# Kernel optimization log

Hardware: AMD Instinct MI355X
Metric: run time of the kernel (lower is better)

## Reference

```python
import jax, jax.numpy as jnp
import numpy as np

B, D, P = 1024, 1024, 16  # batch, latent_dim(=out_dim), part_dim

def setup_inputs() -> dict:
    key = jax.random.key(0)
    k1, k2 = jax.random.split(key)
    x = jax.random.normal(k1, (B, D, P), dtype=jnp.float32)
    # per-part Linear weights, torch Linear weight shape [out, in] stacked over parts
    W = jax.random.normal(k2, (P, D, D), dtype=jnp.float32) * 0.02
    return {"x": x, "W": W}

def reference(x, W):
    # x: [B, D, P]; W: [P, O, D] (O == D here). stack_dim=-1: slice last dim,
    # apply part-specific Linear (no bias) + exact GELU, stack on last dim.
    y = jnp.einsum('bdp,pod->bop', x, W)  # grouped per-part GEMM -> [B, O, P]
    return jax.nn.gelu(y, approximate=False)
```

## Files before the change

### kernel.cpp

```cpp
#include <hip/hip_runtime.h>
#include <hip/hip_bf16.h>
#include <math.h>

typedef __hip_bfloat16 bf16;
typedef __attribute__((ext_vector_type(8))) short bf16x8;
typedef __attribute__((ext_vector_type(4))) float f32x4;

#define DI static __device__ __forceinline__

constexpr int NB = 1024;
constexpr int ND = 1024;
constexpr int NP = 16;
constexpr int BK = 32;

DI float gelu_exact(float x) {
    return 0.5f * x * (1.0f + erff(x * 0.70710678118654752f));
}

__global__ __launch_bounds__(256) void pack_x_kernel(const float* __restrict__ x,
                                                     bf16* __restrict__ xp) {
    const int b = blockIdx.x;
    const int t = threadIdx.x;
    const int p = t & 15;
    const int dg = t >> 4;
    const float* xb = x + (size_t)b * ND * NP;
    bf16* dst = xp + (size_t)p * NB * ND + (size_t)b * ND;
#pragma unroll
    for (int c = 0; c < 8; ++c) {
        const int d0 = dg * 64 + c * 8;
        alignas(16) bf16 tmp[8];
#pragma unroll
        for (int j = 0; j < 8; ++j)
            tmp[j] = __float2bfloat16(xb[(size_t)(d0 + j) * NP + p]);
        *reinterpret_cast<bf16x8*>(&dst[d0]) = *reinterpret_cast<const bf16x8*>(tmp);
    }
}

__global__ __launch_bounds__(256) void pack_w_kernel(const float* __restrict__ w,
                                                     bf16* __restrict__ wp) {
    const size_t i = ((size_t)blockIdx.x * 256 + threadIdx.x) * 8;
    const float4 f0 = *reinterpret_cast<const float4*>(&w[i]);
    const float4 f1 = *reinterpret_cast<const float4*>(&w[i + 4]);
    alignas(16) bf16 tmp[8] = { __float2bfloat16(f0.x), __float2bfloat16(f0.y),
                                __float2bfloat16(f0.z), __float2bfloat16(f0.w),
                                __float2bfloat16(f1.x), __float2bfloat16(f1.y),
                                __float2bfloat16(f1.z), __float2bfloat16(f1.w) };
    *reinterpret_cast<bf16x8*>(&wp[i]) = *reinterpret_cast<const bf16x8*>(tmp);
}

template<bool DIRECT>
__global__ __launch_bounds__(256, 2) void gemm_kernel(const bf16* __restrict__ xp,
                                                      const bf16* __restrict__ wp,
                                                      float* __restrict__ yout) {
    __shared__ bf16 As[2][128 * BK];
    __shared__ bf16 Bs[2][128 * BK];
    const int p  = blockIdx.z;
    const int bt = blockIdx.y * 128;
    const int ot = blockIdx.x * 128;
    const bf16* A  = xp + (size_t)p * NB * ND;
    const bf16* Bm = wp + (size_t)p * ND * ND;
    const int t = threadIdx.x;
    const int l = t & 63;
    const int w = t >> 6;
    const int wr = w >> 1, wc = w & 1;

    f32x4 acc[4][4] = {};

    auto stage = [&](int buf, int k0) {
#pragma unroll
        for (int r = 0; r < 2; ++r) {
            const int c   = r * 256 + t;
            const int row = c >> 2;
            const int cc  = c & 3;
            const bf16* ga = A  + (size_t)(bt + row) * ND + (k0 + cc * 8);
            const bf16* gb = Bm + (size_t)(ot + row) * ND + (k0 + cc * 8);
            bf16* la = &As[buf][(r * 256 + w * 64) * 8];
            bf16* lb = &Bs[buf][(r * 256 + w * 64) * 8];
            __builtin_amdgcn_global_load_lds((const __attribute__((address_space(1))) void*)ga,
                                             (__attribute__((address_space(3))) void*)la, 16, 0, 0);
            __builtin_amdgcn_global_load_lds((const __attribute__((address_space(1))) void*)gb,
                                             (__attribute__((address_space(3))) void*)lb, 16, 0, 0);
        }
    };

    int buf = 0;
    stage(0, 0);
    const int NK = ND / BK;
    for (int kt = 0; kt < NK; ++kt) {
        __syncthreads();
        if (kt + 1 < NK) stage(buf ^ 1, (kt + 1) * BK);
        const int lr = l & 15;
        const int lk = (l >> 4) * 8;
        bf16x8 af[4], bf_[4];
#pragma unroll
        for (int m = 0; m < 4; ++m)
            af[m] = *reinterpret_cast<const bf16x8*>(&As[buf][(wr * 64 + m * 16 + lr) * BK + lk]);
#pragma unroll
        for (int n = 0; n < 4; ++n)
            bf_[n] = *reinterpret_cast<const bf16x8*>(&Bs[buf][(wc * 64 + n * 16 + lr) * BK + lk]);
#pragma unroll
        for (int m = 0; m < 4; ++m)
#pragma unroll
            for (int n = 0; n < 4; ++n)
                acc[m][n] = __builtin_amdgcn_mfma_f32_16x16x32_bf16(af[m], bf_[n], acc[m][n], 0, 0, 0);
        buf ^= 1;
    }

    const int lr4 = (l >> 4) * 4;
    const int lc  = l & 15;
    const int row0 = bt + wr * 64, col0 = ot + wc * 64;
#pragma unroll
    for (int m = 0; m < 4; ++m) {
#pragma unroll
        for (int j = 0; j < 4; ++j) {
            const int r = row0 + m * 16 + lr4 + j;
#pragma unroll
            for (int n = 0; n < 4; ++n) {
                const int c = col0 + n * 16 + lc;
                const float v = acc[m][n][j];
                if (DIRECT) {
                    yout[((size_t)r * ND + c) * NP + p] = gelu_exact(v);
                } else {
                    yout[(size_t)p * NB * ND + (size_t)r * ND + c] = v;
                }
            }
        }
    }
}

__global__ __launch_bounds__(256) void unpack_gelu_kernel(const float* __restrict__ y,
                                                          float* __restrict__ out) {
    const size_t f = (size_t)blockIdx.x * 256 + threadIdx.x;
    const int    p0 = (int)(f & 3) * 4;
    const size_t o  = (f >> 2) & 1023;
    const size_t b  = f >> 12;
    const float* yb = y + b * (size_t)ND + o;
    float4 v;
    v.x = gelu_exact(yb[(size_t)(p0 + 0) * (NB * ND)]);
    v.y = gelu_exact(yb[(size_t)(p0 + 1) * (NB * ND)]);
    v.z = gelu_exact(yb[(size_t)(p0 + 2) * (NB * ND)]);
    v.w = gelu_exact(yb[(size_t)(p0 + 3) * (NB * ND)]);
    reinterpret_cast<float4*>(out)[f] = v;
}

__global__ __launch_bounds__(256) void fallback_kernel(const float* __restrict__ x,
                                                       const float* __restrict__ w,
                                                       float* __restrict__ out) {
    __shared__ float As[64][17];
    __shared__ float Bs[64][17];
    const int p = blockIdx.z, bt = blockIdx.y * 64, ot = blockIdx.x * 64;
    const int t = threadIdx.x;
    const int tx = t & 15, ty = t >> 4;
    float acc[4][4] = {};
    for (int k0 = 0; k0 < ND; k0 += 16) {
        __syncthreads();
#pragma unroll
        for (int i = 0; i < 4; ++i) {
            const int idx = i * 256 + t;
            const int r = idx >> 4, k = idx & 15;
            As[r][k] = x[((size_t)(bt + r) * ND + k0 + k) * NP + p];
            Bs[r][k] = w[(size_t)p * ND * ND + (size_t)(ot + r) * ND + k0 + k];
        }
        __syncthreads();
#pragma unroll
        for (int k = 0; k < 16; ++k) {
            float a[4], bb[4];
#pragma unroll
            for (int i = 0; i < 4; ++i) a[i] = As[ty * 4 + i][k];
#pragma unroll
            for (int j = 0; j < 4; ++j) bb[j] = Bs[tx * 4 + j][k];
#pragma unroll
            for (int i = 0; i < 4; ++i)
#pragma unroll
                for (int j = 0; j < 4; ++j) acc[i][j] += a[i] * bb[j];
        }
    }
#pragma unroll
    for (int i = 0; i < 4; ++i)
#pragma unroll
        for (int j = 0; j < 4; ++j)
            out[((size_t)(bt + ty * 4 + i) * ND + (ot + tx * 4 + j)) * NP + p] =
                gelu_exact(acc[i][j]);
}

extern "C" void kernel_launch(void* const* d_in, const int* in_sizes, int n_in,
                              void* d_out, int out_size, void* d_ws, size_t ws_size,
                              hipStream_t stream) {
    const float* x = (const float*)d_in[0];
    const float* w = (const float*)d_in[1];
    float* out = (float*)d_out;

    const size_t nElem     = (size_t)NP * NB * ND;
    const size_t packBytes = nElem * sizeof(bf16) * 2;
    const size_t yBytes    = nElem * sizeof(float);

    if (ws_size >= packBytes) {
        bf16* xp = (bf16*)d_ws;
        bf16* wp = xp + nElem;
        pack_x_kernel<<<NB, 256, 0, stream>>>(x, xp);
        pack_w_kernel<<<(int)(nElem / (256 * 8)), 256, 0, stream>>>(w, wp);
        if (ws_size >= packBytes + yBytes) {
            float* y = (float*)((char*)d_ws + packBytes);
            gemm_kernel<false><<<dim3(8, 8, 16), 256, 0, stream>>>(xp, wp, y);
            unpack_gelu_kernel<<<(int)(nElem / (256 * 4)), 256, 0, stream>>>(y, out);
        } else {
            gemm_kernel<true><<<dim3(8, 8, 16), 256, 0, stream>>>(xp, wp, out);
        }
    } else {
        fallback_kernel<<<dim3(16, 16, 16), 256, 0, stream>>>(x, w, out);
    }
}
```

Before: 134.8 us.

## Fuse GELU into GEMM, store bf16 intermediate, remap block order, raise occupancy

Moves the exact GELU into the GEMM epilogue and writes the intermediate as bf16 instead of fp32, halving the bytes the GEMM writes and the unpack kernel reads. The grid is flattened to 1D with a remap that interleaves parts across consecutive blocks, presumably to spread L2/channel traffic, and launch bounds are raised to 4 blocks per CU. The bf16 intermediate adds an extra rounding of the output, and the higher occupancy target may force register spills.

```diff
diff --git a/kernel.cpp b/kernel.cpp
--- a/kernel.cpp
+++ b/kernel.cpp
@@ -48,15 +48,17 @@
     *reinterpret_cast<bf16x8*>(&wp[i]) = *reinterpret_cast<const bf16x8*>(tmp);
 }
 
-template<bool DIRECT>
-__global__ __launch_bounds__(256, 2) void gemm_kernel(const bf16* __restrict__ xp,
+template<bool YBF>
+__global__ __launch_bounds__(256, 4) void gemm_kernel(const bf16* __restrict__ xp,
                                                       const bf16* __restrict__ wp,
-                                                      float* __restrict__ yout) {
+                                                      void* __restrict__ yout) {
     __shared__ bf16 As[2][128 * BK];
     __shared__ bf16 Bs[2][128 * BK];
-    const int p  = blockIdx.z;
-    const int bt = blockIdx.y * 128;
-    const int ot = blockIdx.x * 128;
+    const int i = blockIdx.x;
+    const int p    = ((i & 7) << 1) | ((i >> 9) & 1);
+    const int tile = (i >> 3) & 63;
+    const int ot = (tile & 7) * 128;
+    const int bt = (tile >> 3) * 128;
     const bf16* A  = xp + (size_t)p * NB * ND;
     const bf16* Bm = wp + (size_t)p * ND * ND;
     const int t = threadIdx.x;
@@ -117,29 +119,30 @@
 #pragma unroll
             for (int n = 0; n < 4; ++n) {
                 const int c = col0 + n * 16 + lc;
-                const float v = acc[m][n][j];
-                if (DIRECT) {
-                    yout[((size_t)r * ND + c) * NP + p] = gelu_exact(v);
+                const float v = gelu_exact(acc[m][n][j]);
+                if (YBF) {
+                    ((bf16*)yout)[(size_t)p * NB * ND + (size_t)r * ND + c] =
+                        __float2bfloat16(v);
                 } else {
-                    yout[(size_t)p * NB * ND + (size_t)r * ND + c] = v;
+                    ((float*)yout)[((size_t)r * ND + c) * NP + p] = v;
                 }
             }
         }
     }
 }
 
-__global__ __launch_bounds__(256) void unpack_gelu_kernel(const float* __restrict__ y,
-                                                          float* __restrict__ out) {
+__global__ __launch_bounds__(256) void unpack_kernel(const bf16* __restrict__ y,
+                                                     float* __restrict__ out) {
     const size_t f = (size_t)blockIdx.x * 256 + threadIdx.x;
     const int    p0 = (int)(f & 3) * 4;
     const size_t o  = (f >> 2) & 1023;
     const size_t b  = f >> 12;
-    const float* yb = y + b * (size_t)ND + o;
+    const bf16* yb = y + b * (size_t)ND + o;
     float4 v;
-    v.x = gelu_exact(yb[(size_t)(p0 + 0) * (NB * ND)]);
-    v.y = gelu_exact(yb[(size_t)(p0 + 1) * (NB * ND)]);
-    v.z = gelu_exact(yb[(size_t)(p0 + 2) * (NB * ND)]);
-    v.w = gelu_exact(yb[(size_t)(p0 + 3) * (NB * ND)]);
+    v.x = __bfloat162float(yb[(size_t)(p0 + 0) * (NB * ND)]);
+    v.y = __bfloat162float(yb[(size_t)(p0 + 1) * (NB * ND)]);
+    v.z = __bfloat162float(yb[(size_t)(p0 + 2) * (NB * ND)]);
+    v.w = __bfloat162float(yb[(size_t)(p0 + 3) * (NB * ND)]);
     reinterpret_cast<float4*>(out)[f] = v;
 }
 
@@ -192,7 +195,7 @@
 
     const size_t nElem     = (size_t)NP * NB * ND;
     const size_t packBytes = nElem * sizeof(bf16) * 2;
-    const size_t yBytes    = nElem * sizeof(float);
+    const size_t yBytes    = nElem * sizeof(bf16);
 
     if (ws_size >= packBytes) {
         bf16* xp = (bf16*)d_ws;
@@ -200,11 +203,11 @@
         pack_x_kernel<<<NB, 256, 0, stream>>>(x, xp);
         pack_w_kernel<<<(int)(nElem / (256 * 8)), 256, 0, stream>>>(w, wp);
         if (ws_size >= packBytes + yBytes) {
-            float* y = (float*)((char*)d_ws + packBytes);
-            gemm_kernel<false><<<dim3(8, 8, 16), 256, 0, stream>>>(xp, wp, y);
-            unpack_gelu_kernel<<<(int)(nElem / (256 * 4)), 256, 0, stream>>>(y, out);
+            bf16* y = (bf16*)((char*)d_ws + packBytes);
+            gemm_kernel<true><<<1024, 256, 0, stream>>>(xp, wp, y);
+            unpack_kernel<<<(int)(nElem / (256 * 4)), 256, 0, stream>>>(y, out);
         } else {
-            gemm_kernel<true><<<dim3(8, 8, 16), 256, 0, stream>>>(xp, wp, out);
+            gemm_kernel<false><<<1024, 256, 0, stream>>>(xp, wp, out);
         }
     } else {
         fallback_kernel<<<dim3(16, 16, 16), 256, 0, stream>>>(x, w, out);
```

Result: faster. 122.3 us (-9.2%).
